# Kernel optimization log

Measured on AMD Instinct MI355X. Metric: run time of the kernel, lower is better.

The kernel has to match this reference:

```python
import jax, jax.numpy as jnp
import numpy as np

IMG = 256      # image size implied by 8x8 grid * scale 32
THRE = 0.5
DIS = 4        # img_dislocate_size
B = 64


def _shift_map(s, size, dis):
    # Pixel-level coordinate map for the dislocated half: cell r starts at
    # max(r*s - dis, 0) (the torch while-loop clamps negative coords to 0).
    p = jnp.arange(size)
    base = jnp.maximum((p // s) * s - dis, 0)
    return base + p % s


def _cell_norm(x, g, s):
    # Per-cell (crop) min/max normalization, matching the per-crop
    # (t - min) / (max - min + 1e-5) in HeatMaptoImg.
    b = x.shape[0]
    v = x.reshape(b, 1, g, s, g, s)
    mn = v.min(axis=(3, 5), keepdims=True)
    mx = v.max(axis=(3, 5), keepdims=True)
    return ((v - mn) / (mx - mn + 1e-5)).reshape(b, 1, g * s, g * s)


def setup_inputs() -> dict:
    key = jax.random.key(0)
    ks = jax.random.split(key, 7)
    B2 = 2 * B
    return {
        "img": jax.random.uniform(ks[0], (B, 1, IMG, IMG), jnp.float32),
        "heat8": jax.random.uniform(ks[1], (B2, 1, 8, 8), jnp.float32),
        "heat16": jax.random.uniform(ks[2], (B2, 1, 16, 16), jnp.float32),
        "heat32": jax.random.uniform(ks[3], (B2, 1, 32, 32), jnp.float32),
        "seg8": jax.random.uniform(ks[4], (B2, 1, IMG, IMG), jnp.float32),
        "seg16": jax.random.uniform(ks[5], (B2, 1, IMG, IMG), jnp.float32),
        "seg32": jax.random.uniform(ks[6], (B2, 1, IMG, IMG), jnp.float32),
    }


def reference(img, heat8, heat16, heat32, seg8, seg16, seg32):
    Bv = img.shape[0]
    label = jnp.zeros((Bv, 1, IMG, IMG), img.dtype)
    cnt = jnp.zeros_like(label)
    crops = {}
    # fine grid (scale 8) processed first, matching the reversed loop order
    for heat, seg, g in ((heat32, seg32, 32), (heat16, seg16, 16), (heat8, seg8, 8)):
        s = IMG // g                      # crop / cell size for this scale
        mask = (heat > THRE).astype(img.dtype)          # (2B,1,g,g)
        mask_pix = jnp.repeat(jnp.repeat(mask, s, axis=2), s, axis=3)  # (2B,1,256,256)
        Y = _shift_map(s, IMG, DIS)
        # dislocated half crops come from the shifted image region
        img_d = img[:, :, Y[:, None], Y[None, :]]       # (B,1,256,256)
        both = jnp.concatenate([img, img_d], axis=0)    # (2B,1,256,256)
        crops[g] = _cell_norm(both, g, s) * mask_pix
        # UnitLabels: scatter-add per-crop labels + counts, then average
        ca = mask_pix[:Bv]
        label = label + ca * seg[:Bv]
        cnt = cnt + ca
        cd = mask_pix[Bv:]
        label = label.at[:, :, Y[:, None], Y[None, :]].add(cd * seg[Bv:])
        cnt = cnt.at[:, :, Y[:, None], Y[None, :]].add(cd)
    label = label / (cnt + 1e-10)
    return (crops[32], crops[16], crops[8], label)
```

## Files before the change

kernel.cpp:

```cpp
#include <hip/hip_runtime.h>

#define IMG   256
#define IMG2  65536
#define NB    64
#define NB2   128


__device__ __forceinline__ float4 norm4(float4 a, float mn, float inv) {
    float4 o;
    o.x = (a.x - mn) * inv; o.y = (a.y - mn) * inv;
    o.z = (a.z - mn) * inv; o.w = (a.w - mn) * inv;
    return o;
}

__device__ __forceinline__ void mm4(float4 a, float& mn, float& mx) {
    mn = fminf(mn, fminf(fminf(a.x, a.y), fminf(a.z, a.w)));
    mx = fmaxf(mx, fmaxf(fmaxf(a.x, a.y), fmaxf(a.z, a.w)));
}

__device__ __forceinline__ void crops_s8(
    const float* __restrict__ img, const float* __restrict__ heat,
    float* __restrict__ out, int wid) {
    const int l   = threadIdx.x & 63;
    const int src = wid >> 8;
    const int rem = wid & 255;
    const int ci  = rem >> 3;
    const int st  = rem & 7;

    const int r    = l >> 3;
    const int cj   = st * 4 + ((l >> 1) & 3);
    const int o    = (l & 1) * 4;
    const int rowA = ci * 8 + r;
    const int rowB = ((ci == 0) ? 0 : ci * 8 - 4) + r;
    const int colA = st * 32 + (l & 7) * 4;
    const int colB = ((cj == 0) ? 0 : cj * 8 - 4) + o;

    const float* __restrict__ sp = img + (size_t)src * IMG2;
    const float4 a  = *(const float4*)(sp + rowA * IMG + colA);
    const float4 bq = *(const float4*)(sp + rowB * IMG + colB);

    float mnA = 3.4e38f, mxA = -3.4e38f, mnB = 3.4e38f, mxB = -3.4e38f;
    mm4(a, mnA, mxA); mm4(bq, mnB, mxB);
#pragma unroll
    for (int k = 0; k < 4; ++k) {
        const int off = (k == 0) ? 1 : (4 << k);
        mnA = fminf(mnA, __shfl_xor(mnA, off, 64));
        mxA = fmaxf(mxA, __shfl_xor(mxA, off, 64));
        mnB = fminf(mnB, __shfl_xor(mnB, off, 64));
        mxB = fmaxf(mxB, __shfl_xor(mxB, off, 64));
    }
    const float hA = heat[(size_t)src * 1024 + ci * 32 + cj];
    const float hB = heat[(size_t)(src + NB) * 1024 + ci * 32 + cj];
    const float invA = (hA > 0.5f ? 1.0f : 0.0f) / (mxA - mnA + 1e-5f);
    const float invB = (hB > 0.5f ? 1.0f : 0.0f) / (mxB - mnB + 1e-5f);

    const size_t p = (size_t)src * IMG2 + rowA * IMG + colA;
    *(float4*)(out + p)                      = norm4(a,  mnA, invA);
    *(float4*)(out + p + (size_t)NB * IMG2)  = norm4(bq, mnB, invB);
}

__device__ __forceinline__ void crops_s16(
    const float* __restrict__ img, const float* __restrict__ heat,
    float* __restrict__ out, int wid) {
    const int l   = threadIdx.x & 63;
    const int src = wid >> 8;
    const int rem = wid & 255;
    const int ci  = rem >> 4;
    const int cj  = rem & 15;

    const int r    = l >> 2;
    const int o    = (l & 3) * 4;
    const int rowA = ci * 16 + r;
    const int rowB = ((ci == 0) ? 0 : ci * 16 - 4) + r;
    const int colA = cj * 16 + o;
    const int colB = ((cj == 0) ? 0 : cj * 16 - 4) + o;

    const float* __restrict__ sp = img + (size_t)src * IMG2;
    const float4 a  = *(const float4*)(sp + rowA * IMG + colA);
    const float4 bq = *(const float4*)(sp + rowB * IMG + colB);

    float mnA = 3.4e38f, mxA = -3.4e38f, mnB = 3.4e38f, mxB = -3.4e38f;
    mm4(a, mnA, mxA); mm4(bq, mnB, mxB);
#pragma unroll
    for (int off = 1; off < 64; off <<= 1) {
        mnA = fminf(mnA, __shfl_xor(mnA, off, 64));
        mxA = fmaxf(mxA, __shfl_xor(mxA, off, 64));
        mnB = fminf(mnB, __shfl_xor(mnB, off, 64));
        mxB = fmaxf(mxB, __shfl_xor(mxB, off, 64));
    }
    const float hA = heat[(size_t)src * 256 + ci * 16 + cj];
    const float hB = heat[(size_t)(src + NB) * 256 + ci * 16 + cj];
    const float invA = (hA > 0.5f ? 1.0f : 0.0f) / (mxA - mnA + 1e-5f);
    const float invB = (hB > 0.5f ? 1.0f : 0.0f) / (mxB - mnB + 1e-5f);

    const size_t p = (size_t)src * IMG2 + rowA * IMG + colA;
    *(float4*)(out + p)                      = norm4(a,  mnA, invA);
    *(float4*)(out + p + (size_t)NB * IMG2)  = norm4(bq, mnB, invB);
}

__device__ __forceinline__ void crops_s32(
    const float* __restrict__ img, const float* __restrict__ heat,
    float* __restrict__ out, int wid) {
    const int l   = threadIdx.x & 63;
    const int src = wid >> 6;
    const int rem = wid & 63;
    const int ci  = rem >> 3;
    const int cj  = rem & 7;

    const int r0   = l >> 3;
    const int o    = (l & 7) * 4;
    const int rA   = ci * 32;
    const int rB   = (ci == 0) ? 0 : rA - 4;
    const int colA = cj * 32 + o;
    const int colB = ((cj == 0) ? 0 : cj * 32 - 4) + o;

    const float* __restrict__ sp = img + (size_t)src * IMG2;
    float4 a[4], bq[4];
#pragma unroll
    for (int k = 0; k < 4; ++k) {
        const int r = r0 + 8 * k;
        a[k]  = *(const float4*)(sp + (rA + r) * IMG + colA);
        bq[k] = *(const float4*)(sp + (rB + r) * IMG + colB);
    }
    float mnA = 3.4e38f, mxA = -3.4e38f, mnB = 3.4e38f, mxB = -3.4e38f;
#pragma unroll
    for (int k = 0; k < 4; ++k) { mm4(a[k], mnA, mxA); mm4(bq[k], mnB, mxB); }
#pragma unroll
    for (int off = 1; off < 64; off <<= 1) {
        mnA = fminf(mnA, __shfl_xor(mnA, off, 64));
        mxA = fmaxf(mxA, __shfl_xor(mxA, off, 64));
        mnB = fminf(mnB, __shfl_xor(mnB, off, 64));
        mxB = fmaxf(mxB, __shfl_xor(mxB, off, 64));
    }
    const float hA = heat[(size_t)src * 64 + ci * 8 + cj];
    const float hB = heat[(size_t)(src + NB) * 64 + ci * 8 + cj];
    const float invA = (hA > 0.5f ? 1.0f : 0.0f) / (mxA - mnA + 1e-5f);
    const float invB = (hB > 0.5f ? 1.0f : 0.0f) / (mxB - mnB + 1e-5f);

    float* __restrict__ dA = out + (size_t)src * IMG2;
    float* __restrict__ dB = out + (size_t)(src + NB) * IMG2;
#pragma unroll
    for (int k = 0; k < 4; ++k) {
        const int r = r0 + 8 * k;
        *(float4*)(dA + (rA + r) * IMG + colA) = norm4(a[k],  mnA, invA);
        *(float4*)(dB + (rA + r) * IMG + colA) = norm4(bq[k], mnB, invB);
    }
}

__device__ __forceinline__ void label_rows(
    const float* __restrict__ heat8,
    const float* __restrict__ heat16,
    const float* __restrict__ heat32,
    const float* __restrict__ seg8,
    const float* __restrict__ seg16,
    const float* __restrict__ seg32,
    float* __restrict__ out,
    int b, int u0) {
    const int wave = threadIdx.x >> 6;
    const int lane = threadIdx.x & 63;
    const int u    = u0 + wave;
    const int v0   = lane << 2;
    const int vs   = min(v0 + 4, 252);

    float nu[4] = {0.f, 0.f, 0.f, 0.f};
    float de[4] = {0.f, 0.f, 0.f, 0.f};

    if (u0 >= 32 && u0 <= 248) {
        const int i1 = u + 4;
#define SCALE_F(heat, seg, g, l, s)                                           \
        {                                                                     \
            const float* __restrict__ h1 = heat + b * (g * g);                \
            const float* __restrict__ h2 = heat + (NB + b) * (g * g);         \
            const float* __restrict__ r1 = seg + (size_t)b * IMG2 + u * IMG;  \
            const float* __restrict__ r2 =                                    \
                seg + (size_t)(NB + b) * IMG2 + i1 * IMG;                     \
            const float4 sd  = *(const float4*)(r1 + v0);                     \
            const float4 sg0 = *(const float4*)(r2 + v0);                     \
            const float4 sg1 = *(const float4*)(r2 + vs);                     \
            const float hd  = h1[(u >> l) * g + (v0 >> l)];                   \
            const float hg0 = h2[(i1 >> l) * g + (v0 >> l)];                  \
            const float hg1 = h2[(i1 >> l) * g + (vs >> l)];                  \
            const float md = (hd > 0.5f) ? 1.0f : 0.0f;                       \
            const float g0 = (hg0 > 0.5f) ? 1.0f : 0.0f;                      \
            const float g1 = (hg1 > 0.5f) ? 1.0f : 0.0f;                      \
            _Pragma("unroll")                                                 \
            for (int c = 0; c < 4; ++c) {                                     \
                const int v = v0 + c;                                         \
                const float m0 = (v < (s)) ? g0 : 0.0f;                       \
                const float m1 = (v >= (s) - 4 && v <= 251) ? g1 : 0.0f;      \
                float x = ((const float*)&sd)[c] * md;                        \
                x = fmaf(m0, ((const float*)&sg0)[c], x);                     \
                x = fmaf(m1, ((const float*)&sg1)[c], x);                     \
                nu[c] += x;                                                   \
                de[c] += md + m0 + m1;                                        \
            }                                                                 \
        }
        SCALE_F(heat32, seg32, 32, 3, 8)
        SCALE_F(heat16, seg16, 16, 4, 16)
        SCALE_F(heat8,  seg8,  8,  5, 32)
#undef SCALE_F
    } else {
        const int i0  = u;
        const int i1c = min(u + 4, 255);
#define SCALE_G(heat, seg, g, l, s)                                           \
        {                                                                     \
            const float* __restrict__ h1 = heat + b * (g * g);                \
            const float* __restrict__ h2 = heat + (NB + b) * (g * g);         \
            const float* __restrict__ r1 = seg + (size_t)b * IMG2 + u * IMG;  \
            const float* __restrict__ ra =                                    \
                seg + (size_t)(NB + b) * IMG2 + i0 * IMG;                     \
            const float* __restrict__ rb =                                    \
                seg + (size_t)(NB + b) * IMG2 + i1c * IMG;                    \
            const float4 sd  = *(const float4*)(r1 + v0);                     \
            const float4 a0q = *(const float4*)(ra + v0);                     \
            const float4 a1q = *(const float4*)(ra + vs);                     \
            const float4 b0q = *(const float4*)(rb + v0);                     \
            const float4 b1q = *(const float4*)(rb + vs);                     \
            const float hd  = h1[(u >> l) * g + (v0 >> l)];                   \
            const float hA0 = h2[(i0 >> l) * g + (v0 >> l)];                  \
            const float hA1 = h2[(i0 >> l) * g + (vs >> l)];                  \
            const float hB0 = h2[(i1c >> l) * g + (v0 >> l)];                 \
            const float hB1 = h2[(i1c >> l) * g + (vs >> l)];                 \
            const float miA = (u < (s)) ? 1.0f : 0.0f;                        \
            const float miB = (u >= (s) - 4 && u <= 251) ? 1.0f : 0.0f;       \
            const float md  = (hd > 0.5f) ? 1.0f : 0.0f;                      \
            const float gA0 = miA * ((hA0 > 0.5f) ? 1.0f : 0.0f);             \
            const float gA1 = miA * ((hA1 > 0.5f) ? 1.0f : 0.0f);             \
            const float gB0 = miB * ((hB0 > 0.5f) ? 1.0f : 0.0f);             \
            const float gB1 = miB * ((hB1 > 0.5f) ? 1.0f : 0.0f);             \
            _Pragma("unroll")                                                 \
            for (int c = 0; c < 4; ++c) {                                     \
                const int v = v0 + c;                                         \
                const float mj0 = (v < (s)) ? 1.0f : 0.0f;                    \
                const float mj1 = (v >= (s) - 4 && v <= 251) ? 1.0f : 0.0f;   \
                const float w00 = gA0 * mj0, w01 = gA1 * mj1;                 \
                const float w10 = gB0 * mj0, w11 = gB1 * mj1;                 \
                float x = ((const float*)&sd)[c] * md;                        \
                x = fmaf(w00, ((const float*)&a0q)[c], x);                    \
                x = fmaf(w01, ((const float*)&a1q)[c], x);                    \
                x = fmaf(w10, ((const float*)&b0q)[c], x);                    \
                x = fmaf(w11, ((const float*)&b1q)[c], x);                    \
                nu[c] += x;                                                   \
                de[c] += md + w00 + w01 + w10 + w11;                          \
            }                                                                 \
        }
        SCALE_G(heat32, seg32, 32, 3, 8)
        SCALE_G(heat16, seg16, 16, 4, 16)
        SCALE_G(heat8,  seg8,  8,  5, 32)
#undef SCALE_G
    }

    float4 o;
    o.x = nu[0] / (de[0] + 1e-10f);
    o.y = nu[1] / (de[1] + 1e-10f);
    o.z = nu[2] / (de[2] + 1e-10f);
    o.w = nu[3] / (de[3] + 1e-10f);
    *(float4*)(out + (size_t)b * IMG2 + u * IMG + v0) = o;
}

__global__ __launch_bounds__(256) void crops_kernel(
    const float* __restrict__ img,
    const float* __restrict__ heat8,
    const float* __restrict__ heat16,
    const float* __restrict__ heat32,
    float* __restrict__ out) {
    float* crops32 = out;
    float* crops16 = out + (size_t)NB2 * IMG2;
    float* crops8  = out + (size_t)2 * NB2 * IMG2;

    const int cb  = blockIdx.x;
    const int wid = cb * 4 + (threadIdx.x >> 6);
    if (cb < 4096) {
        crops_s8(img, heat32, crops32, wid);
    } else if (cb < 8192) {
        crops_s16(img, heat16, crops16, wid - 16384);
    } else {
        crops_s32(img, heat8, crops8, wid - 32768);
    }
}

__global__ __launch_bounds__(256) void label_kernel(
    const float* __restrict__ heat8,
    const float* __restrict__ heat16,
    const float* __restrict__ heat32,
    const float* __restrict__ seg8,
    const float* __restrict__ seg16,
    const float* __restrict__ seg32,
    float* __restrict__ out) {
    float* label = out + (size_t)3 * NB2 * IMG2;
    const int t  = blockIdx.x;
    label_rows(heat8, heat16, heat32, seg8, seg16, seg32, label,
               t >> 6, (t & 63) << 2);
}

extern "C" void kernel_launch(void* const* d_in, const int* in_sizes, int n_in,
                              void* d_out, int out_size, void* d_ws, size_t ws_size,
                              hipStream_t stream) {
    const float* img    = (const float*)d_in[0];
    const float* heat8  = (const float*)d_in[1];
    const float* heat16 = (const float*)d_in[2];
    const float* heat32 = (const float*)d_in[3];
    const float* seg8   = (const float*)d_in[4];
    const float* seg16  = (const float*)d_in[5];
    const float* seg32  = (const float*)d_in[6];

    label_kernel<<<dim3(4096), 256, 0, stream>>>(
        heat8, heat16, heat32, seg8, seg16, seg32, (float*)d_out);
    crops_kernel<<<dim3(9216), 256, 0, stream>>>(
        img, heat8, heat16, heat32, (float*)d_out);
}
```

Measured before the change: 223.7 us.

## Give each wave more work in crop and label kernels, cutting grid sizes

Each wave in the scale-8 crop path now handles a full cell row (8 strips) and loads its heat values once through a packed per-lane load with shuffles. The scale-16 path handles four cells per wave and batches all loads before reducing. The label kernel now computes two rows per wave, so the interior case reuses index math, and launch bounds request 4 blocks per CU. Grids shrink from 9216/4096 blocks to 2560/2048 blocks, trading fewer launched waves and more memory-level parallelism per wave for higher register pressure and less total parallelism.

```diff
diff --git a/kernel.cpp b/kernel.cpp
--- a/kernel.cpp
+++ b/kernel.cpp
@@ -22,80 +22,111 @@
     const float* __restrict__ img, const float* __restrict__ heat,
     float* __restrict__ out, int wid) {
     const int l   = threadIdx.x & 63;
-    const int src = wid >> 8;
-    const int rem = wid & 255;
-    const int ci  = rem >> 3;
-    const int st  = rem & 7;
-
-    const int r    = l >> 3;
-    const int cj   = st * 4 + ((l >> 1) & 3);
-    const int o    = (l & 1) * 4;
+    const int src = wid >> 5;
+    const int ci  = wid & 31;
+
+    const int r   = l >> 3;
+    const int c8  = l & 7;
+    const int sub = (l >> 1) & 3;
+    const int o   = (l & 1) * 4;
     const int rowA = ci * 8 + r;
     const int rowB = ((ci == 0) ? 0 : ci * 8 - 4) + r;
-    const int colA = st * 32 + (l & 7) * 4;
-    const int colB = ((cj == 0) ? 0 : cj * 8 - 4) + o;
-
-    const float* __restrict__ sp = img + (size_t)src * IMG2;
-    const float4 a  = *(const float4*)(sp + rowA * IMG + colA);
-    const float4 bq = *(const float4*)(sp + rowB * IMG + colB);
-
-    float mnA = 3.4e38f, mxA = -3.4e38f, mnB = 3.4e38f, mxB = -3.4e38f;
-    mm4(a, mnA, mxA); mm4(bq, mnB, mxB);
-#pragma unroll
-    for (int k = 0; k < 4; ++k) {
-        const int off = (k == 0) ? 1 : (4 << k);
-        mnA = fminf(mnA, __shfl_xor(mnA, off, 64));
-        mxA = fmaxf(mxA, __shfl_xor(mxA, off, 64));
-        mnB = fminf(mnB, __shfl_xor(mnB, off, 64));
-        mxB = fmaxf(mxB, __shfl_xor(mxB, off, 64));
-    }
-    const float hA = heat[(size_t)src * 1024 + ci * 32 + cj];
-    const float hB = heat[(size_t)(src + NB) * 1024 + ci * 32 + cj];
-    const float invA = (hA > 0.5f ? 1.0f : 0.0f) / (mxA - mnA + 1e-5f);
-    const float invB = (hB > 0.5f ? 1.0f : 0.0f) / (mxB - mnB + 1e-5f);
-
-    const size_t p = (size_t)src * IMG2 + rowA * IMG + colA;
-    *(float4*)(out + p)                      = norm4(a,  mnA, invA);
-    *(float4*)(out + p + (size_t)NB * IMG2)  = norm4(bq, mnB, invB);
+
+    const float* __restrict__ sp  = img + (size_t)src * IMG2;
+    const float* __restrict__ rpA = sp + rowA * IMG;
+    const float* __restrict__ rpB = sp + rowB * IMG;
+    float* __restrict__ dA = out + (size_t)src * IMG2 + rowA * IMG;
+    float* __restrict__ dB = dA + (size_t)NB * IMG2;
+
+    const float hpack =
+        heat[(size_t)(src + ((l >= 32) ? NB : 0)) * 1024 + ci * 32 + (l & 31)];
+
+#pragma unroll
+    for (int h = 0; h < 2; ++h) {
+        float4 a[4], bq[4];
+#pragma unroll
+        for (int k = 0; k < 4; ++k) {
+            const int st   = h * 4 + k;
+            const int cj   = st * 4 + sub;
+            const int colA = st * 32 + c8 * 4;
+            const int colB = ((cj == 0) ? 0 : cj * 8 - 4) + o;
+            a[k]  = *(const float4*)(rpA + colA);
+            bq[k] = *(const float4*)(rpB + colB);
+        }
+#pragma unroll
+        for (int k = 0; k < 4; ++k) {
+            const int st = h * 4 + k;
+            const int cj = st * 4 + sub;
+            float mnA = 3.4e38f, mxA = -3.4e38f, mnB = 3.4e38f, mxB = -3.4e38f;
+            mm4(a[k], mnA, mxA); mm4(bq[k], mnB, mxB);
+#pragma unroll
+            for (int s = 0; s < 4; ++s) {
+                const int off = (s == 0) ? 1 : (4 << s);
+                mnA = fminf(mnA, __shfl_xor(mnA, off, 64));
+                mxA = fmaxf(mxA, __shfl_xor(mxA, off, 64));
+                mnB = fminf(mnB, __shfl_xor(mnB, off, 64));
+                mxB = fmaxf(mxB, __shfl_xor(mxB, off, 64));
+            }
+            const float hA = __shfl(hpack, cj, 64);
+            const float hB = __shfl(hpack, 32 + cj, 64);
+            const float invA = (hA > 0.5f ? 1.0f : 0.0f) / (mxA - mnA + 1e-5f);
+            const float invB = (hB > 0.5f ? 1.0f : 0.0f) / (mxB - mnB + 1e-5f);
+            const int colA = st * 32 + c8 * 4;
+            *(float4*)(dA + colA) = norm4(a[k],  mnA, invA);
+            *(float4*)(dB + colA) = norm4(bq[k], mnB, invB);
+        }
+    }
 }
 
 __device__ __forceinline__ void crops_s16(
     const float* __restrict__ img, const float* __restrict__ heat,
     float* __restrict__ out, int wid) {
     const int l   = threadIdx.x & 63;
-    const int src = wid >> 8;
-    const int rem = wid & 255;
-    const int ci  = rem >> 4;
-    const int cj  = rem & 15;
+    const int src = wid >> 6;
+    const int rem = wid & 63;
+    const int ci  = rem >> 2;
+    const int q   = rem & 3;
 
     const int r    = l >> 2;
     const int o    = (l & 3) * 4;
     const int rowA = ci * 16 + r;
     const int rowB = ((ci == 0) ? 0 : ci * 16 - 4) + r;
-    const int colA = cj * 16 + o;
-    const int colB = ((cj == 0) ? 0 : cj * 16 - 4) + o;
-
-    const float* __restrict__ sp = img + (size_t)src * IMG2;
-    const float4 a  = *(const float4*)(sp + rowA * IMG + colA);
-    const float4 bq = *(const float4*)(sp + rowB * IMG + colB);
-
-    float mnA = 3.4e38f, mxA = -3.4e38f, mnB = 3.4e38f, mxB = -3.4e38f;
-    mm4(a, mnA, mxA); mm4(bq, mnB, mxB);
-#pragma unroll
-    for (int off = 1; off < 64; off <<= 1) {
-        mnA = fminf(mnA, __shfl_xor(mnA, off, 64));
-        mxA = fmaxf(mxA, __shfl_xor(mxA, off, 64));
-        mnB = fminf(mnB, __shfl_xor(mnB, off, 64));
-        mxB = fmaxf(mxB, __shfl_xor(mxB, off, 64));
-    }
-    const float hA = heat[(size_t)src * 256 + ci * 16 + cj];
-    const float hB = heat[(size_t)(src + NB) * 256 + ci * 16 + cj];
-    const float invA = (hA > 0.5f ? 1.0f : 0.0f) / (mxA - mnA + 1e-5f);
-    const float invB = (hB > 0.5f ? 1.0f : 0.0f) / (mxB - mnB + 1e-5f);
-
-    const size_t p = (size_t)src * IMG2 + rowA * IMG + colA;
-    *(float4*)(out + p)                      = norm4(a,  mnA, invA);
-    *(float4*)(out + p + (size_t)NB * IMG2)  = norm4(bq, mnB, invB);
+
+    const float* __restrict__ sp  = img + (size_t)src * IMG2;
+    const float* __restrict__ rpA = sp + rowA * IMG;
+    const float* __restrict__ rpB = sp + rowB * IMG;
+    float* __restrict__ dA = out + (size_t)src * IMG2 + rowA * IMG;
+    float* __restrict__ dB = dA + (size_t)NB * IMG2;
+
+    float4 a[4], bq[4];
+#pragma unroll
+    for (int k = 0; k < 4; ++k) {
+        const int cj   = q * 4 + k;
+        const int colA = cj * 16 + o;
+        const int colB = ((cj == 0) ? 0 : cj * 16 - 4) + o;
+        a[k]  = *(const float4*)(rpA + colA);
+        bq[k] = *(const float4*)(rpB + colB);
+    }
+#pragma unroll
+    for (int k = 0; k < 4; ++k) {
+        const int cj = q * 4 + k;
+        float mnA = 3.4e38f, mxA = -3.4e38f, mnB = 3.4e38f, mxB = -3.4e38f;
+        mm4(a[k], mnA, mxA); mm4(bq[k], mnB, mxB);
+#pragma unroll
+        for (int off = 1; off < 64; off <<= 1) {
+            mnA = fminf(mnA, __shfl_xor(mnA, off, 64));
+            mxA = fmaxf(mxA, __shfl_xor(mxA, off, 64));
+            mnB = fminf(mnB, __shfl_xor(mnB, off, 64));
+            mxB = fmaxf(mxB, __shfl_xor(mxB, off, 64));
+        }
+        const float hA = heat[(size_t)src * 256 + ci * 16 + cj];
+        const float hB = heat[(size_t)(src + NB) * 256 + ci * 16 + cj];
+        const float invA = (hA > 0.5f ? 1.0f : 0.0f) / (mxA - mnA + 1e-5f);
+        const float invB = (hB > 0.5f ? 1.0f : 0.0f) / (mxB - mnB + 1e-5f);
+        const int colA = cj * 16 + o;
+        *(float4*)(dA + colA) = norm4(a[k],  mnA, invA);
+        *(float4*)(dB + colA) = norm4(bq[k], mnB, invB);
+    }
 }
 
 __device__ __forceinline__ void crops_s32(
@@ -147,7 +178,7 @@
     }
 }
 
-__device__ __forceinline__ void label_rows(
+__device__ __forceinline__ void label_row_generic(
     const float* __restrict__ heat8,
     const float* __restrict__ heat16,
     const float* __restrict__ heat32,
@@ -155,101 +186,57 @@
     const float* __restrict__ seg16,
     const float* __restrict__ seg32,
     float* __restrict__ out,
-    int b, int u0) {
-    const int wave = threadIdx.x >> 6;
-    const int lane = threadIdx.x & 63;
-    const int u    = u0 + wave;
-    const int v0   = lane << 2;
-    const int vs   = min(v0 + 4, 252);
-
+    int b, int u, int v0, int vs) {
     float nu[4] = {0.f, 0.f, 0.f, 0.f};
     float de[4] = {0.f, 0.f, 0.f, 0.f};
-
-    if (u0 >= 32 && u0 <= 248) {
-        const int i1 = u + 4;
-#define SCALE_F(heat, seg, g, l, s)                                           \
-        {                                                                     \
-            const float* __restrict__ h1 = heat + b * (g * g);                \
-            const float* __restrict__ h2 = heat + (NB + b) * (g * g);         \
-            const float* __restrict__ r1 = seg + (size_t)b * IMG2 + u * IMG;  \
-            const float* __restrict__ r2 =                                    \
-                seg + (size_t)(NB + b) * IMG2 + i1 * IMG;                     \
-            const float4 sd  = *(const float4*)(r1 + v0);                     \
-            const float4 sg0 = *(const float4*)(r2 + v0);                     \
-            const float4 sg1 = *(const float4*)(r2 + vs);                     \
-            const float hd  = h1[(u >> l) * g + (v0 >> l)];                   \
-            const float hg0 = h2[(i1 >> l) * g + (v0 >> l)];                  \
-            const float hg1 = h2[(i1 >> l) * g + (vs >> l)];                  \
-            const float md = (hd > 0.5f) ? 1.0f : 0.0f;                       \
-            const float g0 = (hg0 > 0.5f) ? 1.0f : 0.0f;                      \
-            const float g1 = (hg1 > 0.5f) ? 1.0f : 0.0f;                      \
-            _Pragma("unroll")                                                 \
-            for (int c = 0; c < 4; ++c) {                                     \
-                const int v = v0 + c;                                         \
-                const float m0 = (v < (s)) ? g0 : 0.0f;                       \
-                const float m1 = (v >= (s) - 4 && v <= 251) ? g1 : 0.0f;      \
-                float x = ((const float*)&sd)[c] * md;                        \
-                x = fmaf(m0, ((const float*)&sg0)[c], x);                     \
-                x = fmaf(m1, ((const float*)&sg1)[c], x);                     \
-                nu[c] += x;                                                   \
-                de[c] += md + m0 + m1;                                        \
-            }                                                                 \
-        }
-        SCALE_F(heat32, seg32, 32, 3, 8)
-        SCALE_F(heat16, seg16, 16, 4, 16)
-        SCALE_F(heat8,  seg8,  8,  5, 32)
-#undef SCALE_F
-    } else {
-        const int i0  = u;
-        const int i1c = min(u + 4, 255);
+    const int i0  = u;
+    const int i1c = min(u + 4, 255);
 #define SCALE_G(heat, seg, g, l, s)                                           \
-        {                                                                     \
-            const float* __restrict__ h1 = heat + b * (g * g);                \
-            const float* __restrict__ h2 = heat + (NB + b) * (g * g);         \
-            const float* __restrict__ r1 = seg + (size_t)b * IMG2 + u * IMG;  \
-            const float* __restrict__ ra =                                    \
-                seg + (size_t)(NB + b) * IMG2 + i0 * IMG;                     \
-            const float* __restrict__ rb =                                    \
-                seg + (size_t)(NB + b) * IMG2 + i1c * IMG;                    \
-            const float4 sd  = *(const float4*)(r1 + v0);                     \
-            const float4 a0q = *(const float4*)(ra + v0);                     \
-            const float4 a1q = *(const float4*)(ra + vs);                     \
-            const float4 b0q = *(const float4*)(rb + v0);                     \
-            const float4 b1q = *(const float4*)(rb + vs);                     \
-            const float hd  = h1[(u >> l) * g + (v0 >> l)];                   \
-            const float hA0 = h2[(i0 >> l) * g + (v0 >> l)];                  \
-            const float hA1 = h2[(i0 >> l) * g + (vs >> l)];                  \
-            const float hB0 = h2[(i1c >> l) * g + (v0 >> l)];                 \
-            const float hB1 = h2[(i1c >> l) * g + (vs >> l)];                 \
-            const float miA = (u < (s)) ? 1.0f : 0.0f;                        \
-            const float miB = (u >= (s) - 4 && u <= 251) ? 1.0f : 0.0f;       \
-            const float md  = (hd > 0.5f) ? 1.0f : 0.0f;                      \
-            const float gA0 = miA * ((hA0 > 0.5f) ? 1.0f : 0.0f);             \
-            const float gA1 = miA * ((hA1 > 0.5f) ? 1.0f : 0.0f);             \
-            const float gB0 = miB * ((hB0 > 0.5f) ? 1.0f : 0.0f);             \
-            const float gB1 = miB * ((hB1 > 0.5f) ? 1.0f : 0.0f);             \
-            _Pragma("unroll")                                                 \
-            for (int c = 0; c < 4; ++c) {                                     \
-                const int v = v0 + c;                                         \
-                const float mj0 = (v < (s)) ? 1.0f : 0.0f;                    \
-                const float mj1 = (v >= (s) - 4 && v <= 251) ? 1.0f : 0.0f;   \
-                const float w00 = gA0 * mj0, w01 = gA1 * mj1;                 \
-                const float w10 = gB0 * mj0, w11 = gB1 * mj1;                 \
-                float x = ((const float*)&sd)[c] * md;                        \
-                x = fmaf(w00, ((const float*)&a0q)[c], x);                    \
-                x = fmaf(w01, ((const float*)&a1q)[c], x);                    \
-                x = fmaf(w10, ((const float*)&b0q)[c], x);                    \
-                x = fmaf(w11, ((const float*)&b1q)[c], x);                    \
-                nu[c] += x;                                                   \
-                de[c] += md + w00 + w01 + w10 + w11;                          \
-            }                                                                 \
-        }
-        SCALE_G(heat32, seg32, 32, 3, 8)
-        SCALE_G(heat16, seg16, 16, 4, 16)
-        SCALE_G(heat8,  seg8,  8,  5, 32)
+    {                                                                         \
+        const float* __restrict__ h1 = heat + b * (g * g);                    \
+        const float* __restrict__ h2 = heat + (NB + b) * (g * g);             \
+        const float* __restrict__ r1 = seg + (size_t)b * IMG2 + u * IMG;      \
+        const float* __restrict__ ra =                                        \
+            seg + (size_t)(NB + b) * IMG2 + i0 * IMG;                         \
+        const float* __restrict__ rb =                                        \
+            seg + (size_t)(NB + b) * IMG2 + i1c * IMG;                        \
+        const float4 sd  = *(const float4*)(r1 + v0);                         \
+        const float4 a0q = *(const float4*)(ra + v0);                         \
+        const float4 a1q = *(const float4*)(ra + vs);                         \
+        const float4 b0q = *(const float4*)(rb + v0);                         \
+        const float4 b1q = *(const float4*)(rb + vs);                         \
+        const float hd  = h1[(u >> l) * g + (v0 >> l)];                       \
+        const float hA0 = h2[(i0 >> l) * g + (v0 >> l)];                      \
+        const float hA1 = h2[(i0 >> l) * g + (vs >> l)];                      \
+        const float hB0 = h2[(i1c >> l) * g + (v0 >> l)];                     \
+        const float hB1 = h2[(i1c >> l) * g + (vs >> l)];                     \
+        const float miA = (u < (s)) ? 1.0f : 0.0f;                            \
+        const float miB = (u >= (s) - 4 && u <= 251) ? 1.0f : 0.0f;           \
+        const float md  = (hd > 0.5f) ? 1.0f : 0.0f;                          \
+        const float gA0 = miA * ((hA0 > 0.5f) ? 1.0f : 0.0f);                 \
+        const float gA1 = miA * ((hA1 > 0.5f) ? 1.0f : 0.0f);                 \
+        const float gB0 = miB * ((hB0 > 0.5f) ? 1.0f : 0.0f);                 \
+        const float gB1 = miB * ((hB1 > 0.5f) ? 1.0f : 0.0f);                 \
+        _Pragma("unroll")                                                     \
+        for (int c = 0; c < 4; ++c) {                                         \
+            const int v = v0 + c;                                             \
+            const float mj0 = (v < (s)) ? 1.0f : 0.0f;                        \
+            const float mj1 = (v >= (s) - 4 && v <= 251) ? 1.0f : 0.0f;       \
+            const float w00 = gA0 * mj0, w01 = gA1 * mj1;                     \
+            const float w10 = gB0 * mj0, w11 = gB1 * mj1;                     \
+            float x = ((const float*)&sd)[c] * md;                            \
+            x = fmaf(w00, ((const float*)&a0q)[c], x);                        \
+            x = fmaf(w01, ((const float*)&a1q)[c], x);                        \
+            x = fmaf(w10, ((const float*)&b0q)[c], x);                        \
+            x = fmaf(w11, ((const float*)&b1q)[c], x);                        \
+            nu[c] += x;                                                       \
+            de[c] += md + w00 + w01 + w10 + w11;                              \
+        }                                                                     \
+    }
+    SCALE_G(heat32, seg32, 32, 3, 8)
+    SCALE_G(heat16, seg16, 16, 4, 16)
+    SCALE_G(heat8,  seg8,  8,  5, 32)
 #undef SCALE_G
-    }
-
     float4 o;
     o.x = nu[0] / (de[0] + 1e-10f);
     o.y = nu[1] / (de[1] + 1e-10f);
@@ -258,7 +245,94 @@
     *(float4*)(out + (size_t)b * IMG2 + u * IMG + v0) = o;
 }
 
-__global__ __launch_bounds__(256) void crops_kernel(
+__global__ __launch_bounds__(256, 4) void label_kernel(
+    const float* __restrict__ heat8,
+    const float* __restrict__ heat16,
+    const float* __restrict__ heat32,
+    const float* __restrict__ seg8,
+    const float* __restrict__ seg16,
+    const float* __restrict__ seg32,
+    float* __restrict__ out) {
+    float* label = out + (size_t)3 * NB2 * IMG2;
+    const int lid  = blockIdx.x * 4 + (threadIdx.x >> 6);
+    const int b    = lid >> 7;
+    const int u    = (lid & 127) << 1;
+    const int lane = threadIdx.x & 63;
+    const int v0   = lane << 2;
+    const int vs   = min(v0 + 4, 252);
+
+    if (u >= 32 && u <= 250) {
+        float nu0[4] = {0.f,0.f,0.f,0.f}, de0[4] = {0.f,0.f,0.f,0.f};
+        float nu1[4] = {0.f,0.f,0.f,0.f}, de1[4] = {0.f,0.f,0.f,0.f};
+#define SCALE_F2(heat, seg, g, l, s)                                          \
+        {                                                                     \
+            const float* __restrict__ h1 = heat + b * (g * g);                \
+            const float* __restrict__ h2 = heat + (NB + b) * (g * g);         \
+            const float* __restrict__ r1 = seg + (size_t)b * IMG2 + u * IMG;  \
+            const float* __restrict__ r2 =                                    \
+                seg + (size_t)(NB + b) * IMG2 + (u + 4) * IMG;                \
+            const float4 sd0 = *(const float4*)(r1 + v0);                     \
+            const float4 sd1 = *(const float4*)(r1 + IMG + v0);               \
+            const float4 g00 = *(const float4*)(r2 + v0);                     \
+            const float4 g10 = *(const float4*)(r2 + vs);                     \
+            const float4 g01 = *(const float4*)(r2 + IMG + v0);               \
+            const float4 g11 = *(const float4*)(r2 + IMG + vs);               \
+            const float hd0  = h1[(u >> l) * g + (v0 >> l)];                  \
+            const float hd1  = h1[((u + 1) >> l) * g + (v0 >> l)];            \
+            const float hg00 = h2[((u + 4) >> l) * g + (v0 >> l)];            \
+            const float hg10 = h2[((u + 4) >> l) * g + (vs >> l)];            \
+            const float hg01 = h2[((u + 5) >> l) * g + (v0 >> l)];            \
+            const float hg11 = h2[((u + 5) >> l) * g + (vs >> l)];            \
+            const float md0 = (hd0 > 0.5f) ? 1.0f : 0.0f;                     \
+            const float md1 = (hd1 > 0.5f) ? 1.0f : 0.0f;                     \
+            const float q00 = (hg00 > 0.5f) ? 1.0f : 0.0f;                    \
+            const float q10 = (hg10 > 0.5f) ? 1.0f : 0.0f;                    \
+            const float q01 = (hg01 > 0.5f) ? 1.0f : 0.0f;                    \
+            const float q11 = (hg11 > 0.5f) ? 1.0f : 0.0f;                    \
+            _Pragma("unroll")                                                 \
+            for (int c = 0; c < 4; ++c) {                                     \
+                const int v = v0 + c;                                         \
+                const float mj0 = (v < (s)) ? 1.0f : 0.0f;                    \
+                const float mj1 = (v >= (s) - 4 && v <= 251) ? 1.0f : 0.0f;   \
+                const float m00 = mj0 * q00, m10 = mj1 * q10;                 \
+                const float m01 = mj0 * q01, m11 = mj1 * q11;                 \
+                float x0 = ((const float*)&sd0)[c] * md0;                     \
+                x0 = fmaf(m00, ((const float*)&g00)[c], x0);                  \
+                x0 = fmaf(m10, ((const float*)&g10)[c], x0);                  \
+                nu0[c] += x0;                                                 \
+                de0[c] += md0 + m00 + m10;                                    \
+                float x1 = ((const float*)&sd1)[c] * md1;                     \
+                x1 = fmaf(m01, ((const float*)&g01)[c], x1);                  \
+                x1 = fmaf(m11, ((const float*)&g11)[c], x1);                  \
+                nu1[c] += x1;                                                 \
+                de1[c] += md1 + m01 + m11;                                    \
+            }                                                                 \
+        }
+        SCALE_F2(heat32, seg32, 32, 3, 8)
+        SCALE_F2(heat16, seg16, 16, 4, 16)
+        SCALE_F2(heat8,  seg8,  8,  5, 32)
+#undef SCALE_F2
+        float4 o0, o1;
+        o0.x = nu0[0] / (de0[0] + 1e-10f);
+        o0.y = nu0[1] / (de0[1] + 1e-10f);
+        o0.z = nu0[2] / (de0[2] + 1e-10f);
+        o0.w = nu0[3] / (de0[3] + 1e-10f);
+        o1.x = nu1[0] / (de1[0] + 1e-10f);
+        o1.y = nu1[1] / (de1[1] + 1e-10f);
+        o1.z = nu1[2] / (de1[2] + 1e-10f);
+        o1.w = nu1[3] / (de1[3] + 1e-10f);
+        float* p = label + (size_t)b * IMG2 + u * IMG + v0;
+        *(float4*)p         = o0;
+        *(float4*)(p + IMG) = o1;
+    } else {
+        label_row_generic(heat8, heat16, heat32, seg8, seg16, seg32, label,
+                          b, u,     v0, vs);
+        label_row_generic(heat8, heat16, heat32, seg8, seg16, seg32, label,
+                          b, u + 1, v0, vs);
+    }
+}
+
+__global__ __launch_bounds__(256, 4) void crops_kernel(
     const float* __restrict__ img,
     const float* __restrict__ heat8,
     const float* __restrict__ heat16,
@@ -268,29 +342,15 @@
     float* crops16 = out + (size_t)NB2 * IMG2;
     float* crops8  = out + (size_t)2 * NB2 * IMG2;
 
-    const int cb  = blockIdx.x;
-    const int wid = cb * 4 + (threadIdx.x >> 6);
-    if (cb < 4096) {
-        crops_s8(img, heat32, crops32, wid);
-    } else if (cb < 8192) {
-        crops_s16(img, heat16, crops16, wid - 16384);
+    const int cb = blockIdx.x;
+    const int w  = threadIdx.x >> 6;
+    if (cb < 512) {
+        crops_s8(img, heat32, crops32, cb * 4 + w);
+    } else if (cb < 1536) {
+        crops_s16(img, heat16, crops16, (cb - 512) * 4 + w);
     } else {
-        crops_s32(img, heat8, crops8, wid - 32768);
-    }
-}
-
-__global__ __launch_bounds__(256) void label_kernel(
-    const float* __restrict__ heat8,
-    const float* __restrict__ heat16,
-    const float* __restrict__ heat32,
-    const float* __restrict__ seg8,
-    const float* __restrict__ seg16,
-    const float* __restrict__ seg32,
-    float* __restrict__ out) {
-    float* label = out + (size_t)3 * NB2 * IMG2;
-    const int t  = blockIdx.x;
-    label_rows(heat8, heat16, heat32, seg8, seg16, seg32, label,
-               t >> 6, (t & 63) << 2);
+        crops_s32(img, heat8, crops8, (cb - 1536) * 4 + w);
+    }
 }
 
 extern "C" void kernel_launch(void* const* d_in, const int* in_sizes, int n_in,
@@ -304,8 +364,8 @@
     const float* seg16  = (const float*)d_in[5];
     const float* seg32  = (const float*)d_in[6];
 
-    label_kernel<<<dim3(4096), 256, 0, stream>>>(
+    label_kernel<<<dim3(2048), 256, 0, stream>>>(
         heat8, heat16, heat32, seg8, seg16, seg32, (float*)d_out);
-    crops_kernel<<<dim3(9216), 256, 0, stream>>>(
+    crops_kernel<<<dim3(2560), 256, 0, stream>>>(
         img, heat8, heat16, heat32, (float*)d_out);
 }
```

After: 233.8 us. 1.05x slower.
